# Performance work log

Measured on AMD Instinct MI355X. Metric: run time of the kernel, lower is better.

The kernel has to match this reference:

```python
import jax, jax.numpy as jnp
import numpy as np

B, L, DS, DP = 4, 384, 384, 128
NEAR_BAND = 4
LN_EPS = 1e-5


def setup_inputs():
    key = jax.random.key(0)
    k = jax.random.split(key, 16)
    return {
        "seq_repr": jax.random.normal(k[0], (B, L, DS), jnp.float32),
        "pair_repr": jax.random.normal(k[1], (B, L, L, DP), jnp.float32),
        "ln_s_g": 1.0 + 0.1 * jax.random.normal(k[2], (DS,), jnp.float32),
        "ln_s_b": 0.1 * jax.random.normal(k[3], (DS,), jnp.float32),
        "ln_z_g": 1.0 + 0.1 * jax.random.normal(k[4], (DP,), jnp.float32),
        "ln_z_b": 0.1 * jax.random.normal(k[5], (DP,), jnp.float32),
        "W_seq": jax.random.normal(k[6], (DS, DS), jnp.float32) / np.sqrt(DS).astype(np.float32),
        "W_pair": jax.random.normal(k[7], (DP, DP), jnp.float32) / np.sqrt(DP).astype(np.float32),
        "W_gs": 0.02 * jax.random.normal(k[8], (2 * DS, DS), jnp.float32),
        "b_gs": jnp.ones((DS,), jnp.float32),
        "W_gz": 0.02 * jax.random.normal(k[9], (2 * DP, DP), jnp.float32),
        "b_gz": jnp.ones((DP,), jnp.float32),
        "W1": jax.random.normal(k[10], (DS + 2 * DP, 64), jnp.float32) / np.sqrt(DS + 2 * DP).astype(np.float32),
        "b1": 0.01 * jax.random.normal(k[11], (64,), jnp.float32),
        "W2": jax.random.normal(k[12], (64, 1), jnp.float32) / 8.0,
        "b2": jnp.zeros((1,), jnp.float32),
        "chain_id": jax.random.randint(k[13], (B, L), 0, 2, jnp.int32),
        "mask": jax.random.randint(k[14], (B, L), 0, 2, jnp.int32).astype(jnp.bool_),
    }


def _layernorm(x, g, b):
    mu = jnp.mean(x, axis=-1, keepdims=True)
    var = jnp.mean(jnp.square(x - mu), axis=-1, keepdims=True)
    return (x - mu) * jax.lax.rsqrt(var + LN_EPS) * g + b


def _masked_mean(x, m, axes):
    num = jnp.sum(x * m, axis=axes)
    den = jnp.clip(jnp.sum(m, axis=axes), 1e-6, None)  # mask has trailing dim 1 -> den broadcasts
    return num / den


def _masked_max(x, m, axis):
    v = jnp.max(jnp.where(m > 0, x, -jnp.inf), axis=axis)
    return jnp.where(jnp.isinf(v), jnp.zeros_like(v), v)


def reference(seq_repr, pair_repr, ln_s_g, ln_s_b, ln_z_g, ln_z_b, W_seq, W_pair,
              W_gs, b_gs, W_gz, b_gz, W1, b1, W2, b2, chain_id, mask):
    # sequence branch: LN -> Linear -> masked mean/max over L -> gated blend
    s = _layernorm(seq_repr, ln_s_g, ln_s_b) @ W_seq          # [B,L,DS]
    m = mask.astype(s.dtype)[..., None]                        # [B,L,1]
    s_mean = _masked_mean(s, m, 1)                             # [B,DS]
    s_max = _masked_max(s, m, 1)                               # [B,DS]
    gate_s = jax.nn.sigmoid(jnp.concatenate([s_max, s_mean], -1) @ W_gs + b_gs)
    s_feat = s_mean + gate_s * (s_max - s_mean)

    # pair branch: symmetrize, zero diagonal, LN -> Linear
    p = 0.5 * (pair_repr + jnp.swapaxes(pair_repr, 1, 2))      # [B,L,L,DP]
    eye = jnp.eye(L, dtype=p.dtype)[None, :, :, None]
    p = p * (1.0 - eye)
    p = _layernorm(p, ln_z_g, ln_z_b) @ W_pair

    pm = (mask[:, :, None] & mask[:, None, :])[..., None].astype(p.dtype)   # [B,L,L,1]
    same = (chain_id[:, :, None] == chain_id[:, None, :])[..., None]
    intra = pm * same.astype(p.dtype)
    inter = pm * (~same).astype(p.dtype)

    inter_mean = _masked_mean(p, inter, (1, 2))                # [B,DP]
    row_den = jnp.clip(jnp.sum(inter, axis=2), 1e-6, None)     # [B,L,1]
    row_mean = jnp.sum(p * inter, axis=2) / row_den            # [B,L,DP]
    inter_peak = jnp.max(row_mean, axis=1)                     # [B,DP]
    gate_z = jax.nn.sigmoid(jnp.concatenate([inter_peak, inter_mean], -1) @ W_gz + b_gz)
    inter_feat = inter_mean + gate_z * (inter_peak - inter_mean)

    idx = jnp.arange(L)
    band = (jnp.abs(idx[:, None] - idx[None, :]) <= NEAR_BAND)[None, :, :, None].astype(p.dtype)
    intra_compact = _masked_mean(p, intra * band, (1, 2))      # [B,DP]

    feat = jnp.concatenate([s_feat, inter_feat, intra_compact], -1)  # [B, DS+2*DP]
    h = jax.nn.relu(feat @ W1 + b1)
    prob = jax.nn.sigmoid(h @ W2 + b2)[..., 0]                 # [B]
    return prob
```

## Files before the change

kernel.cpp:

```cpp
#include <hip/hip_runtime.h>
#include <math.h>

#define B_  4
#define L_  384
#define DS_ 384
#define DP_ 128
#define NB_ 4
#define FEAT_ (DS_ + 2*DP_)
#define LN_EPS_ 1e-5f
#define T_ 16
#define NT_ (L_ / T_)
#define NTP_ (NT_ * (NT_ + 1) / 2)
#define SROWS_ 4

__device__ __forceinline__ int detect_mode_block(const void* __restrict__ raw) {
    const unsigned int* dw = (const unsigned int*)raw;
    int li = 1, lf = 1;
    for (int i = threadIdx.x; i < (B_ * L_) / 4; i += blockDim.x) {
        unsigned int v = dw[i];
        if (v != 0u && v != 1u) li = 0;
        if (v != 0u && v != 0x3F800000u) lf = 0;
    }
    int ai = __syncthreads_and(li);
    int af = __syncthreads_and(lf);
    return ai ? 0 : (af ? 1 : 2);
}
__device__ __forceinline__ int mask_at(const void* __restrict__ raw, int mode, int idx) {
    if (mode == 0) return ((const unsigned int*)raw)[idx] != 0u;
    if (mode == 1) return ((const float*)raw)[idx] != 0.0f;
    return ((const unsigned char*)raw)[idx] != 0;
}

__device__ __forceinline__ size_t poff(int b, int tile, int slot, int row) {
    return ((((size_t)b * NT_ + tile) * NT_ + slot) * T_ + row) * DP_;
}
__device__ __forceinline__ size_t pdoff(int b, int tile, int slot, int row) {
    return (((size_t)b * NT_ + tile) * NT_ + slot) * T_ + row;
}

__global__ __launch_bounds__(256) void k_pair_tiles(
    const float* __restrict__ pair, const float* __restrict__ gz,
    const float* __restrict__ bz, const int* __restrict__ chain,
    const void* __restrict__ mask_raw,
    float* __restrict__ PI, float* __restrict__ PA,
    float* __restrict__ PDI, float* __restrict__ PDA) {
    __shared__ float smJI[T_][DP_], smJA[T_][DP_];
    __shared__ float smDJI[T_], smDJA[T_];
    __shared__ int s_m[2 * T_], s_c[2 * T_];

    const int mode = detect_mode_block(mask_raw);

    const int b = blockIdx.x / NTP_;
    int t = blockIdx.x % NTP_;
    int ta = 0;
    while (t >= NT_ - ta) { t -= NT_ - ta; ta++; }
    const int tb = ta + t;
    const int i0 = ta * T_, j0 = tb * T_;
    const float fac = (ta == tb) ? 0.5f : 1.0f;

    const int tid = threadIdx.x;
    const int wave = tid >> 6, lane = tid & 63;
    const int ch2 = lane * 2;

    for (int idx = tid; idx < T_ * DP_; idx += 256) {
        (&smJI[0][0])[idx] = 0.f;
        (&smJA[0][0])[idx] = 0.f;
    }
    if (tid < T_) { smDJI[tid] = 0.f; smDJA[tid] = 0.f; }
    if (tid < 2 * T_) {
        const int loc = (tid < T_) ? (i0 + tid) : (j0 + tid - T_);
        s_m[tid] = mask_at(mask_raw, mode, b * L_ + loc);
        s_c[tid] = chain[b * L_ + loc];
    }
    __syncthreads();

    const float g0 = gz[ch2], g1 = gz[ch2 + 1];
    const float bb0 = bz[ch2], bb1 = bz[ch2 + 1];
    const float* baseb = pair + (size_t)b * L_ * L_ * DP_;

    float accI0[4] = {0, 0, 0, 0}, accI1[4] = {0, 0, 0, 0};
    float accA0[4] = {0, 0, 0, 0}, accA1[4] = {0, 0, 0, 0};
    float denI[4] = {0, 0, 0, 0}, denA[4] = {0, 0, 0, 0};

    for (int r = 0; r < 4; ++r) {
        const int il = (wave << 2) + r;
        const int gi = i0 + il;
        if (!s_m[il]) continue;
        const int ci = s_c[il];
        for (int jl = 0; jl < T_; ++jl) {
            if (!s_m[T_ + jl]) continue;
            const int gj = j0 + jl;
            const bool same = (s_c[T_ + jl] == ci);
            int d = gi - gj; d = d < 0 ? -d : d;
            const float wI = (!same) ? fac : 0.f;
            const float wA = (same && d <= NB_) ? fac : 0.f;
            if (wI == 0.f && wA == 0.f) continue;
            float v0, v1;
            if (gi == gj) {
                v0 = 0.f; v1 = 0.f;
            } else {
                const float2 a = *(const float2*)(baseb + ((size_t)gi * L_ + gj) * DP_ + ch2);
                const float2 c = *(const float2*)(baseb + ((size_t)gj * L_ + gi) * DP_ + ch2);
                v0 = 0.5f * (a.x + c.x); v1 = 0.5f * (a.y + c.y);
            }
            float s = v0 + v1, q = v0 * v0 + v1 * v1;
            #pragma unroll
            for (int off = 32; off; off >>= 1) {
                s += __shfl_xor(s, off);
                q += __shfl_xor(q, off);
            }
            const float mu = s * (1.f / DP_);
            const float rstd = rsqrtf(q * (1.f / DP_) - mu * mu + LN_EPS_);
            const float y0 = (v0 - mu) * rstd * g0 + bb0;
            const float y1 = (v1 - mu) * rstd * g1 + bb1;
            accI0[r] += wI * y0; accI1[r] += wI * y1;
            accA0[r] += wA * y0; accA1[r] += wA * y1;
            denI[r] += wI; denA[r] += wA;
            if (wI != 0.f) {
                atomicAdd(&smJI[jl][ch2], wI * y0);
                atomicAdd(&smJI[jl][ch2 + 1], wI * y1);
                if (lane == 0) atomicAdd(&smDJI[jl], wI);
            }
            if (wA != 0.f) {
                atomicAdd(&smJA[jl][ch2], wA * y0);
                atomicAdd(&smJA[jl][ch2 + 1], wA * y1);
                if (lane == 0) atomicAdd(&smDJA[jl], wA);
            }
        }
    }
    __syncthreads();

    if (ta != tb) {
        #pragma unroll
        for (int r = 0; r < 4; ++r) {
            const int il = (wave << 2) + r;
            const size_t o = poff(b, ta, tb, il) + ch2;
            PI[o] = accI0[r]; PI[o + 1] = accI1[r];
            PA[o] = accA0[r]; PA[o + 1] = accA1[r];
            if (lane == 0) {
                PDI[pdoff(b, ta, tb, il)] = denI[r];
                PDA[pdoff(b, ta, tb, il)] = denA[r];
            }
        }
        for (int idx = tid; idx < T_ * DP_; idx += 256) {
            const int jl = idx >> 7, ch = idx & 127;
            const size_t o = poff(b, tb, ta, jl) + ch;
            PI[o] = smJI[jl][ch];
            PA[o] = smJA[jl][ch];
        }
        if (tid < T_) {
            PDI[pdoff(b, tb, ta, tid)] = smDJI[tid];
            PDA[pdoff(b, tb, ta, tid)] = smDJA[tid];
        }
    } else {
        #pragma unroll
        for (int r = 0; r < 4; ++r) {
            const int il = (wave << 2) + r;
            const size_t o = poff(b, ta, ta, il) + ch2;
            PI[o] = accI0[r] + smJI[il][ch2];
            PI[o + 1] = accI1[r] + smJI[il][ch2 + 1];
            PA[o] = accA0[r] + smJA[il][ch2];
            PA[o + 1] = accA1[r] + smJA[il][ch2 + 1];
            if (lane == 0) {
                PDI[pdoff(b, ta, ta, il)] = denI[r] + smDJI[il];
                PDA[pdoff(b, ta, ta, il)] = denA[r] + smDJA[il];
            }
        }
    }
}

__global__ __launch_bounds__(384) void k_seq_proj(
    const float* __restrict__ seq, const float* __restrict__ gs,
    const float* __restrict__ bs, const float* __restrict__ W,
    float* __restrict__ s_rows) {
    const int row0 = blockIdx.x * SROWS_;
    const int tid = threadIdx.x;
    const int wave = tid >> 6, lane = tid & 63;
    __shared__ float xn[SROWS_][DS_];
    __shared__ float sSum[SROWS_][6], sSq[SROWS_][6];
    const float gg = gs[tid], bbv = bs[tid];
    #pragma unroll
    for (int r = 0; r < SROWS_; r++) {
        float x = seq[(size_t)(row0 + r) * DS_ + tid];
        float s = x, q = x * x;
        #pragma unroll
        for (int off = 32; off; off >>= 1) {
            s += __shfl_xor(s, off);
            q += __shfl_xor(q, off);
        }
        if (lane == 0) { sSum[r][wave] = s; sSq[r][wave] = q; }
        xn[r][tid] = x;
    }
    __syncthreads();
    float mu[SROWS_], rstd[SROWS_];
    #pragma unroll
    for (int r = 0; r < SROWS_; r++) {
        float ts = 0.f, tq = 0.f;
        #pragma unroll
        for (int w = 0; w < 6; w++) { ts += sSum[r][w]; tq += sSq[r][w]; }
        mu[r] = ts * (1.0f / DS_);
        float var = tq * (1.0f / DS_) - mu[r] * mu[r];
        rstd[r] = rsqrtf(var + LN_EPS_);
    }
    #pragma unroll
    for (int r = 0; r < SROWS_; r++)
        xn[r][tid] = (xn[r][tid] - mu[r]) * rstd[r] * gg + bbv;
    __syncthreads();
    float acc[SROWS_] = {0.f, 0.f, 0.f, 0.f};
    for (int k = 0; k < DS_; k++) {
        float w = W[(size_t)k * DS_ + tid];
        #pragma unroll
        for (int r = 0; r < SROWS_; r++) acc[r] += xn[r][k] * w;
    }
    #pragma unroll
    for (int r = 0; r < SROWS_; r++)
        s_rows[(size_t)(row0 + r) * DS_ + tid] = acc[r];
}

__global__ __launch_bounds__(384) void k_mid(
    const float* __restrict__ s_rows, const void* __restrict__ mask_raw,
    const float* __restrict__ Wp,
    const float* __restrict__ PI, const float* __restrict__ PA,
    const float* __restrict__ PDI, const float* __restrict__ PDA,
    float* __restrict__ psum, float* __restrict__ pmax, int* __restrict__ pcnt,
    float* __restrict__ pI, float* __restrict__ pA, float* __restrict__ pPk,
    float* __restrict__ pdI, float* __restrict__ pdA) {
    __shared__ float sWp[DP_ * DP_];
    __shared__ float sRS[DP_];
    const int tid = threadIdx.x;

    if (blockIdx.x < B_ * NT_) {
        const int b = blockIdx.x / NT_, tile = blockIdx.x % NT_;
        for (int i = tid; i < DP_ * DP_; i += 384) sWp[i] = Wp[i];
        __syncthreads();
        float totI = 0.f, totA = 0.f, dI = 0.f, dA = 0.f, peak = -INFINITY;
        for (int r = 0; r < T_; ++r) {
            float dr = 0.f;
            if (tid < DP_) {
                float rsI = 0.f, rsA = 0.f, da = 0.f;
                const size_t o0 = poff(b, tile, 0, r) + tid;
                const size_t d0 = pdoff(b, tile, 0, r);
                #pragma unroll 4
                for (int s = 0; s < NT_; ++s) {
                    rsI += PI[o0 + (size_t)s * T_ * DP_];
                    rsA += PA[o0 + (size_t)s * T_ * DP_];
                    dr += PDI[d0 + (size_t)s * T_];
                    da += PDA[d0 + (size_t)s * T_];
                }
                sRS[tid] = rsI;
                totI += rsI; totA += rsA; dI += dr; dA += da;
            }
            __syncthreads();
            if (tid < DP_) {
                float acc = 0.f;
                #pragma unroll 8
                for (int k = 0; k < DP_; ++k) acc += sRS[k] * sWp[(k << 7) + tid];
                peak = fmaxf(peak, acc / fmaxf(dr, 1e-6f));
            }
            __syncthreads();
        }
        if (tid < DP_) {
            pI[(size_t)(b * NT_ + tile) * DP_ + tid] = totI;
            pA[(size_t)(b * NT_ + tile) * DP_ + tid] = totA;
            pPk[(size_t)(b * NT_ + tile) * DP_ + tid] = peak;
            if (tid == 0) { pdI[b * NT_ + tile] = dI; pdA[b * NT_ + tile] = dA; }
        }
    } else {
        const int bi = blockIdx.x - B_ * NT_;
        const int b = bi / NT_, tile = bi % NT_;
        const int mode = detect_mode_block(mask_raw);
        float sum = 0.f, mx = -INFINITY;
        int cnt = 0;
        const int l0 = tile * T_;
        for (int l = l0; l < l0 + T_; ++l) {
            if (mask_at(mask_raw, mode, b * L_ + l)) {
                float v = s_rows[(size_t)(b * L_ + l) * DS_ + tid];
                sum += v; mx = fmaxf(mx, v); cnt++;
            }
        }
        psum[(size_t)(b * NT_ + tile) * DS_ + tid] = sum;
        pmax[(size_t)(b * NT_ + tile) * DS_ + tid] = mx;
        if (tid == 0) pcnt[b * NT_ + tile] = cnt;
    }
}

__global__ __launch_bounds__(384) void k_finalize(
    const float* __restrict__ psum, const float* __restrict__ pmax,
    const int* __restrict__ pcnt,
    const float* __restrict__ pI, const float* __restrict__ pA,
    const float* __restrict__ pPk,
    const float* __restrict__ pdI, const float* __restrict__ pdA,
    const float* __restrict__ Wgs, const float* __restrict__ bgs,
    const float* __restrict__ Wp, const float* __restrict__ Wgz,
    const float* __restrict__ bgz,
    const float* __restrict__ W1, const float* __restrict__ b1,
    const float* __restrict__ W2, const float* __restrict__ b2,
    float* __restrict__ out) {
    const int b = blockIdx.x;
    const int tid = threadIdx.x;
    __shared__ float sMean[DS_], sMax[DS_], fI[DP_], fA[DP_], sPk[DP_], sIM[DP_];
    __shared__ float feat[FEAT_];
    __shared__ float sdI, sdA;
    {
        float s = 0.f, m = -INFINITY;
        int cnt = 0;
        for (int c = 0; c < NT_; ++c) {
            s += psum[(size_t)(b * NT_ + c) * DS_ + tid];
            m = fmaxf(m, pmax[(size_t)(b * NT_ + c) * DS_ + tid]);
            cnt += pcnt[b * NT_ + c];
        }
        sMean[tid] = s / fmaxf((float)cnt, 1e-6f);
        sMax[tid] = (cnt > 0) ? m : 0.f;
    }
    if (tid < DP_) {
        float tI = 0.f, tA = 0.f, pk = -INFINITY, ddI = 0.f, ddA = 0.f;
        for (int c = 0; c < NT_; ++c) {
            tI += pI[(size_t)(b * NT_ + c) * DP_ + tid];
            tA += pA[(size_t)(b * NT_ + c) * DP_ + tid];
            pk = fmaxf(pk, pPk[(size_t)(b * NT_ + c) * DP_ + tid]);
            ddI += pdI[b * NT_ + c]; ddA += pdA[b * NT_ + c];
        }
        fI[tid] = tI; fA[tid] = tA; sPk[tid] = pk;
        if (tid == 0) { sdI = ddI; sdA = ddA; }
    }
    __syncthreads();
    {
        float acc = bgs[tid];
        #pragma unroll 4
        for (int k = 0; k < DS_; ++k)
            acc += sMax[k] * Wgs[(size_t)k * DS_ + tid]
                 + sMean[k] * Wgs[(size_t)(k + DS_) * DS_ + tid];
        const float gate = 1.f / (1.f + expf(-acc));
        feat[tid] = sMean[tid] + gate * (sMax[tid] - sMean[tid]);
    }
    if (tid < DP_) {
        float aI = 0.f, aA = 0.f;
        #pragma unroll 4
        for (int k = 0; k < DP_; ++k) {
            aI += fI[k] * Wp[(k << 7) + tid];
            aA += fA[k] * Wp[(k << 7) + tid];
        }
        sIM[tid] = aI / fmaxf(sdI, 1e-6f);
        feat[DS_ + DP_ + tid] = aA / fmaxf(sdA, 1e-6f);
    }
    __syncthreads();
    if (tid < DP_) {
        float acc = bgz[tid];
        #pragma unroll 4
        for (int k = 0; k < DP_; ++k)
            acc += sPk[k] * Wgz[(k << 7) + tid] + sIM[k] * Wgz[((k + DP_) << 7) + tid];
        const float gate = 1.f / (1.f + expf(-acc));
        feat[DS_ + tid] = sIM[tid] + gate * (sPk[tid] - sIM[tid]);
    }
    __syncthreads();
    if (tid < 64) {
        float acc = b1[tid];
        #pragma unroll 4
        for (int k = 0; k < FEAT_; ++k) acc += feat[k] * W1[(k << 6) + tid];
        float p = fmaxf(acc, 0.f) * W2[tid];
        #pragma unroll
        for (int off = 32; off; off >>= 1) p += __shfl_xor(p, off);
        if (tid == 0) out[b] = 1.f / (1.f + expf(-(p + b2[0])));
    }
}

extern "C" void kernel_launch(void* const* d_in, const int* in_sizes, int n_in,
                              void* d_out, int out_size, void* d_ws, size_t ws_size,
                              hipStream_t stream) {
    const float* seq    = (const float*)d_in[0];
    const float* pair   = (const float*)d_in[1];
    const float* ln_s_g = (const float*)d_in[2];
    const float* ln_s_b = (const float*)d_in[3];
    const float* ln_z_g = (const float*)d_in[4];
    const float* ln_z_b = (const float*)d_in[5];
    const float* W_seq  = (const float*)d_in[6];
    const float* W_pair = (const float*)d_in[7];
    const float* W_gs   = (const float*)d_in[8];
    const float* b_gs   = (const float*)d_in[9];
    const float* W_gz   = (const float*)d_in[10];
    const float* b_gz   = (const float*)d_in[11];
    const float* W1     = (const float*)d_in[12];
    const float* b1     = (const float*)d_in[13];
    const float* W2     = (const float*)d_in[14];
    const float* b2     = (const float*)d_in[15];
    const int*   chain  = (const int*)d_in[16];
    const void*  mask   = d_in[17];
    float* out = (float*)d_out;

    char* ws = (char*)d_ws;
    const size_t nP  = (size_t)B_ * NT_ * NT_ * T_ * DP_;
    const size_t nPD = (size_t)B_ * NT_ * NT_ * T_;
    float* PI  = (float*)ws;  ws += nP * 4;
    float* PA  = (float*)ws;  ws += nP * 4;
    float* PDI = (float*)ws;  ws += nPD * 4;
    float* PDA = (float*)ws;  ws += nPD * 4;
    float* s_rows = (float*)ws; ws += (size_t)B_ * L_ * DS_ * 4;
    float* psum = (float*)ws;   ws += (size_t)B_ * NT_ * DS_ * 4;
    float* pmax = (float*)ws;   ws += (size_t)B_ * NT_ * DS_ * 4;
    int*   pcnt = (int*)ws;     ws += (size_t)B_ * NT_ * 4;
    float* pI   = (float*)ws;   ws += (size_t)B_ * NT_ * DP_ * 4;
    float* pA   = (float*)ws;   ws += (size_t)B_ * NT_ * DP_ * 4;
    float* pPk  = (float*)ws;   ws += (size_t)B_ * NT_ * DP_ * 4;
    float* pdI  = (float*)ws;   ws += (size_t)B_ * NT_ * 4;
    float* pdA  = (float*)ws;   ws += (size_t)B_ * NT_ * 4;

    k_seq_proj<<<(B_ * L_) / SROWS_, 384, 0, stream>>>(seq, ln_s_g, ln_s_b, W_seq, s_rows);
    k_pair_tiles<<<B_ * NTP_, 256, 0, stream>>>(pair, ln_z_g, ln_z_b, chain, mask,
                                                PI, PA, PDI, PDA);
    k_mid<<<2 * B_ * NT_, 384, 0, stream>>>(s_rows, mask, W_pair, PI, PA, PDI, PDA,
                                            psum, pmax, pcnt, pI, pA, pPk, pdI, pdA);
    k_finalize<<<B_, 384, 0, stream>>>(psum, pmax, pcnt, pI, pA, pPk, pdI, pdA,
                                       W_gs, b_gs, W_pair, W_gz, b_gz,
                                       W1, b1, W2, b2, out);
}
```

Baseline: 655.3 us.

## Merge seq projection into pair-tile kernel and batch eligible pair loads via ballot

Combines the sequence LayerNorm+projection and the pair-tile reduction into one launch, with extra blocks handling sequence rows (now 8 rows per 256-thread block). In the pair path, a wave ballot precomputes which (i,j) pairs are eligible, so the loop iterates only those and issues up to four pairs' global loads before their LayerNorm reductions, for more memory-level parallelism. Diagonal tiles now fold row accumulators through shared atomics. The aim is to remove a launch, let the two independent workloads overlap on the GPU, and hide pair-load latency, at the cost of more registers and larger unrolled code.

```diff
diff --git a/kernel.cpp b/kernel.cpp
--- a/kernel.cpp
+++ b/kernel.cpp
@@ -11,7 +11,7 @@
 #define T_ 16
 #define NT_ (L_ / T_)
 #define NTP_ (NT_ * (NT_ + 1) / 2)
-#define SROWS_ 4
+#define SQROWS_ 8
 
 __device__ __forceinline__ int detect_mode_block(const void* __restrict__ raw) {
     const unsigned int* dw = (const unsigned int*)raw;
@@ -38,110 +38,162 @@
     return (((size_t)b * NT_ + tile) * NT_ + slot) * T_ + row;
 }
 
-__global__ __launch_bounds__(256) void k_pair_tiles(
+#define WREDUCE2(S, Q) do { \
+    (S) += __shfl_xor((S), 32); (Q) += __shfl_xor((Q), 32); \
+    (S) += __shfl_xor((S), 16); (Q) += __shfl_xor((Q), 16); \
+    (S) += __shfl_xor((S), 8);  (Q) += __shfl_xor((Q), 8);  \
+    (S) += __shfl_xor((S), 4);  (Q) += __shfl_xor((Q), 4);  \
+    (S) += __shfl_xor((S), 2);  (Q) += __shfl_xor((Q), 2);  \
+    (S) += __shfl_xor((S), 1);  (Q) += __shfl_xor((Q), 1);  \
+} while (0)
+
+#define LNACC(JL, AA, CC) do { \
+    const int gj_ = j0 + (JL); \
+    const bool same_ = (s_c[T_ + (JL)] == ci); \
+    int dd_ = gi - gj_; dd_ = dd_ < 0 ? -dd_ : dd_; \
+    const float wI_ = same_ ? 0.f : fac; \
+    const float wA_ = (same_ && dd_ <= NB_) ? fac : 0.f; \
+    float v0_, v1_; \
+    if (gi == gj_) { v0_ = 0.f; v1_ = 0.f; } \
+    else { v0_ = 0.5f * ((AA).x + (CC).x); v1_ = 0.5f * ((AA).y + (CC).y); } \
+    float s_ = v0_ + v1_, q_ = v0_ * v0_ + v1_ * v1_; \
+    WREDUCE2(s_, q_); \
+    const float mu_ = s_ * (1.f / DP_); \
+    const float rstd_ = rsqrtf(q_ * (1.f / DP_) - mu_ * mu_ + LN_EPS_); \
+    const float y0_ = (v0_ - mu_) * rstd_ * g0 + bb0; \
+    const float y1_ = (v1_ - mu_) * rstd_ * g1 + bb1; \
+    aI0 += wI_ * y0_; aI1 += wI_ * y1_; \
+    aA0 += wA_ * y0_; aA1 += wA_ * y1_; \
+    adI += wI_; adA += wA_; \
+    if (wI_ != 0.f) { \
+        atomicAdd(&smJI[JL][ch2], wI_ * y0_); \
+        atomicAdd(&smJI[JL][ch2 + 1], wI_ * y1_); \
+        if (lane == 0) atomicAdd(&smDJI[JL], wI_); \
+    } \
+    if (wA_ != 0.f) { \
+        atomicAdd(&smJA[JL][ch2], wA_ * y0_); \
+        atomicAdd(&smJA[JL][ch2 + 1], wA_ * y1_); \
+        if (lane == 0) atomicAdd(&smDJA[JL], wA_); \
+    } \
+} while (0)
+
+__global__ __launch_bounds__(256) void k_main(
     const float* __restrict__ pair, const float* __restrict__ gz,
     const float* __restrict__ bz, const int* __restrict__ chain,
     const void* __restrict__ mask_raw,
+    const float* __restrict__ seq, const float* __restrict__ gs,
+    const float* __restrict__ bs, const float* __restrict__ Wseq,
     float* __restrict__ PI, float* __restrict__ PA,
-    float* __restrict__ PDI, float* __restrict__ PDA) {
-    __shared__ float smJI[T_][DP_], smJA[T_][DP_];
-    __shared__ float smDJI[T_], smDJA[T_];
-    __shared__ int s_m[2 * T_], s_c[2 * T_];
-
-    const int mode = detect_mode_block(mask_raw);
-
-    const int b = blockIdx.x / NTP_;
-    int t = blockIdx.x % NTP_;
-    int ta = 0;
-    while (t >= NT_ - ta) { t -= NT_ - ta; ta++; }
-    const int tb = ta + t;
-    const int i0 = ta * T_, j0 = tb * T_;
-    const float fac = (ta == tb) ? 0.5f : 1.0f;
-
+    float* __restrict__ PDI, float* __restrict__ PDA,
+    float* __restrict__ s_rows) {
+    __shared__ __align__(16) float shraw[4200];
     const int tid = threadIdx.x;
     const int wave = tid >> 6, lane = tid & 63;
-    const int ch2 = lane * 2;
-
-    for (int idx = tid; idx < T_ * DP_; idx += 256) {
-        (&smJI[0][0])[idx] = 0.f;
-        (&smJA[0][0])[idx] = 0.f;
-    }
-    if (tid < T_) { smDJI[tid] = 0.f; smDJA[tid] = 0.f; }
-    if (tid < 2 * T_) {
-        const int loc = (tid < T_) ? (i0 + tid) : (j0 + tid - T_);
-        s_m[tid] = mask_at(mask_raw, mode, b * L_ + loc);
-        s_c[tid] = chain[b * L_ + loc];
-    }
-    __syncthreads();
-
-    const float g0 = gz[ch2], g1 = gz[ch2 + 1];
-    const float bb0 = bz[ch2], bb1 = bz[ch2 + 1];
-    const float* baseb = pair + (size_t)b * L_ * L_ * DP_;
-
-    float accI0[4] = {0, 0, 0, 0}, accI1[4] = {0, 0, 0, 0};
-    float accA0[4] = {0, 0, 0, 0}, accA1[4] = {0, 0, 0, 0};
-    float denI[4] = {0, 0, 0, 0}, denA[4] = {0, 0, 0, 0};
-
-    for (int r = 0; r < 4; ++r) {
-        const int il = (wave << 2) + r;
-        const int gi = i0 + il;
-        if (!s_m[il]) continue;
-        const int ci = s_c[il];
-        for (int jl = 0; jl < T_; ++jl) {
-            if (!s_m[T_ + jl]) continue;
-            const int gj = j0 + jl;
-            const bool same = (s_c[T_ + jl] == ci);
-            int d = gi - gj; d = d < 0 ? -d : d;
-            const float wI = (!same) ? fac : 0.f;
-            const float wA = (same && d <= NB_) ? fac : 0.f;
-            if (wI == 0.f && wA == 0.f) continue;
-            float v0, v1;
-            if (gi == gj) {
-                v0 = 0.f; v1 = 0.f;
-            } else {
-                const float2 a = *(const float2*)(baseb + ((size_t)gi * L_ + gj) * DP_ + ch2);
-                const float2 c = *(const float2*)(baseb + ((size_t)gj * L_ + gi) * DP_ + ch2);
-                v0 = 0.5f * (a.x + c.x); v1 = 0.5f * (a.y + c.y);
-            }
-            float s = v0 + v1, q = v0 * v0 + v1 * v1;
-            #pragma unroll
-            for (int off = 32; off; off >>= 1) {
-                s += __shfl_xor(s, off);
-                q += __shfl_xor(q, off);
-            }
-            const float mu = s * (1.f / DP_);
-            const float rstd = rsqrtf(q * (1.f / DP_) - mu * mu + LN_EPS_);
-            const float y0 = (v0 - mu) * rstd * g0 + bb0;
-            const float y1 = (v1 - mu) * rstd * g1 + bb1;
-            accI0[r] += wI * y0; accI1[r] += wI * y1;
-            accA0[r] += wA * y0; accA1[r] += wA * y1;
-            denI[r] += wI; denA[r] += wA;
-            if (wI != 0.f) {
-                atomicAdd(&smJI[jl][ch2], wI * y0);
-                atomicAdd(&smJI[jl][ch2 + 1], wI * y1);
-                if (lane == 0) atomicAdd(&smDJI[jl], wI);
-            }
-            if (wA != 0.f) {
-                atomicAdd(&smJA[jl][ch2], wA * y0);
-                atomicAdd(&smJA[jl][ch2 + 1], wA * y1);
-                if (lane == 0) atomicAdd(&smDJA[jl], wA);
-            }
-        }
-    }
-    __syncthreads();
-
-    if (ta != tb) {
+
+    if (blockIdx.x < B_ * NTP_) {
+        float (*smJI)[DP_] = (float(*)[DP_])shraw;
+        float (*smJA)[DP_] = (float(*)[DP_])(shraw + 2048);
+        float* smDJI = shraw + 4096;
+        float* smDJA = shraw + 4112;
+        int* s_m = (int*)(shraw + 4128);
+        int* s_c = (int*)(shraw + 4160);
+
+        const int mode = detect_mode_block(mask_raw);
+
+        const int b = blockIdx.x / NTP_;
+        int t = blockIdx.x % NTP_;
+        int ta = 0;
+        while (t >= NT_ - ta) { t -= NT_ - ta; ta++; }
+        const int tb = ta + t;
+        const int i0 = ta * T_, j0 = tb * T_;
+        const float fac = (ta == tb) ? 0.5f : 1.0f;
+        const int ch2 = lane * 2;
+
+        for (int idx = tid; idx < T_ * DP_; idx += 256) {
+            (&smJI[0][0])[idx] = 0.f;
+            (&smJA[0][0])[idx] = 0.f;
+        }
+        if (tid < T_) { smDJI[tid] = 0.f; smDJA[tid] = 0.f; }
+        if (tid < 2 * T_) {
+            const int loc = (tid < T_) ? (i0 + tid) : (j0 + tid - T_);
+            s_m[tid] = mask_at(mask_raw, mode, b * L_ + loc);
+            s_c[tid] = chain[b * L_ + loc];
+        }
+        __syncthreads();
+
+        const float g0 = gz[ch2], g1 = gz[ch2 + 1];
+        const float bb0 = bz[ch2], bb1 = bz[ch2 + 1];
+        const float* baseb = pair + (size_t)b * L_ * L_ * DP_;
+
+        unsigned long long elig;
+        {
+            const int r_ = lane >> 4, jl_ = lane & 15;
+            const int il_ = (wave << 2) + r_;
+            bool e = s_m[il_] && s_m[T_ + jl_];
+            if (e) {
+                const bool same = (s_c[T_ + jl_] == s_c[il_]);
+                int dd = (i0 + il_) - (j0 + jl_); dd = dd < 0 ? -dd : dd;
+                e = (!same) || (dd <= NB_);
+            }
+            elig = __ballot(e);
+        }
+
         #pragma unroll
         for (int r = 0; r < 4; ++r) {
             const int il = (wave << 2) + r;
-            const size_t o = poff(b, ta, tb, il) + ch2;
-            PI[o] = accI0[r]; PI[o + 1] = accI1[r];
-            PA[o] = accA0[r]; PA[o + 1] = accA1[r];
-            if (lane == 0) {
-                PDI[pdoff(b, ta, tb, il)] = denI[r];
-                PDA[pdoff(b, ta, tb, il)] = denA[r];
-            }
-        }
+            const int gi = i0 + il;
+            const int ci = s_c[il];
+            float aI0 = 0.f, aI1 = 0.f, aA0 = 0.f, aA1 = 0.f, adI = 0.f, adA = 0.f;
+            unsigned int mr = (unsigned int)((elig >> (r * 16)) & 0xFFFFull);
+            while (mr) {
+                int ja = __ffs(mr) - 1; mr &= mr - 1;
+                int jb = -1, jc = -1, jd = -1;
+                if (mr) { jb = __ffs(mr) - 1; mr &= mr - 1; }
+                if (mr) { jc = __ffs(mr) - 1; mr &= mr - 1; }
+                if (mr) { jd = __ffs(mr) - 1; mr &= mr - 1; }
+                float2 Aa = make_float2(0.f, 0.f), Ca = Aa, Ab = Aa, Cb = Aa;
+                float2 Ac = Aa, Cc = Aa, Ad = Aa, Cd = Aa;
+                if (gi != j0 + ja) {
+                    Aa = *(const float2*)(baseb + ((size_t)gi * L_ + (j0 + ja)) * DP_ + ch2);
+                    Ca = *(const float2*)(baseb + ((size_t)(j0 + ja) * L_ + gi) * DP_ + ch2);
+                }
+                if (jb >= 0 && gi != j0 + jb) {
+                    Ab = *(const float2*)(baseb + ((size_t)gi * L_ + (j0 + jb)) * DP_ + ch2);
+                    Cb = *(const float2*)(baseb + ((size_t)(j0 + jb) * L_ + gi) * DP_ + ch2);
+                }
+                if (jc >= 0 && gi != j0 + jc) {
+                    Ac = *(const float2*)(baseb + ((size_t)gi * L_ + (j0 + jc)) * DP_ + ch2);
+                    Cc = *(const float2*)(baseb + ((size_t)(j0 + jc) * L_ + gi) * DP_ + ch2);
+                }
+                if (jd >= 0 && gi != j0 + jd) {
+                    Ad = *(const float2*)(baseb + ((size_t)gi * L_ + (j0 + jd)) * DP_ + ch2);
+                    Cd = *(const float2*)(baseb + ((size_t)(j0 + jd) * L_ + gi) * DP_ + ch2);
+                }
+                LNACC(ja, Aa, Ca);
+                if (jb >= 0) LNACC(jb, Ab, Cb);
+                if (jc >= 0) LNACC(jc, Ac, Cc);
+                if (jd >= 0) LNACC(jd, Ad, Cd);
+            }
+            if (ta != tb) {
+                const size_t o = poff(b, ta, tb, il) + ch2;
+                PI[o] = aI0; PI[o + 1] = aI1;
+                PA[o] = aA0; PA[o + 1] = aA1;
+                if (lane == 0) {
+                    PDI[pdoff(b, ta, tb, il)] = adI;
+                    PDA[pdoff(b, ta, tb, il)] = adA;
+                }
+            } else {
+                atomicAdd(&smJI[il][ch2], aI0);
+                atomicAdd(&smJI[il][ch2 + 1], aI1);
+                atomicAdd(&smJA[il][ch2], aA0);
+                atomicAdd(&smJA[il][ch2 + 1], aA1);
+                if (lane == 0) {
+                    atomicAdd(&smDJI[il], adI);
+                    atomicAdd(&smDJA[il], adA);
+                }
+            }
+        }
+        __syncthreads();
         for (int idx = tid; idx < T_ * DP_; idx += 256) {
             const int jl = idx >> 7, ch = idx & 127;
             const size_t o = poff(b, tb, ta, jl) + ch;
@@ -153,68 +205,59 @@
             PDA[pdoff(b, tb, ta, tid)] = smDJA[tid];
         }
     } else {
-        #pragma unroll
-        for (int r = 0; r < 4; ++r) {
-            const int il = (wave << 2) + r;
-            const size_t o = poff(b, ta, ta, il) + ch2;
-            PI[o] = accI0[r] + smJI[il][ch2];
-            PI[o + 1] = accI1[r] + smJI[il][ch2 + 1];
-            PA[o] = accA0[r] + smJA[il][ch2];
-            PA[o + 1] = accA1[r] + smJA[il][ch2 + 1];
-            if (lane == 0) {
-                PDI[pdoff(b, ta, ta, il)] = denI[r] + smDJI[il];
-                PDA[pdoff(b, ta, ta, il)] = denA[r] + smDJA[il];
-            }
-        }
-    }
-}
-
-__global__ __launch_bounds__(384) void k_seq_proj(
-    const float* __restrict__ seq, const float* __restrict__ gs,
-    const float* __restrict__ bs, const float* __restrict__ W,
-    float* __restrict__ s_rows) {
-    const int row0 = blockIdx.x * SROWS_;
-    const int tid = threadIdx.x;
-    const int wave = tid >> 6, lane = tid & 63;
-    __shared__ float xn[SROWS_][DS_];
-    __shared__ float sSum[SROWS_][6], sSq[SROWS_][6];
-    const float gg = gs[tid], bbv = bs[tid];
-    #pragma unroll
-    for (int r = 0; r < SROWS_; r++) {
-        float x = seq[(size_t)(row0 + r) * DS_ + tid];
-        float s = x, q = x * x;
-        #pragma unroll
-        for (int off = 32; off; off >>= 1) {
-            s += __shfl_xor(s, off);
-            q += __shfl_xor(q, off);
-        }
-        if (lane == 0) { sSum[r][wave] = s; sSq[r][wave] = q; }
-        xn[r][tid] = x;
-    }
-    __syncthreads();
-    float mu[SROWS_], rstd[SROWS_];
-    #pragma unroll
-    for (int r = 0; r < SROWS_; r++) {
-        float ts = 0.f, tq = 0.f;
-        #pragma unroll
-        for (int w = 0; w < 6; w++) { ts += sSum[r][w]; tq += sSq[r][w]; }
-        mu[r] = ts * (1.0f / DS_);
-        float var = tq * (1.0f / DS_) - mu[r] * mu[r];
-        rstd[r] = rsqrtf(var + LN_EPS_);
-    }
-    #pragma unroll
-    for (int r = 0; r < SROWS_; r++)
-        xn[r][tid] = (xn[r][tid] - mu[r]) * rstd[r] * gg + bbv;
-    __syncthreads();
-    float acc[SROWS_] = {0.f, 0.f, 0.f, 0.f};
-    for (int k = 0; k < DS_; k++) {
-        float w = W[(size_t)k * DS_ + tid];
-        #pragma unroll
-        for (int r = 0; r < SROWS_; r++) acc[r] += xn[r][k] * w;
-    }
-    #pragma unroll
-    for (int r = 0; r < SROWS_; r++)
-        s_rows[(size_t)(row0 + r) * DS_ + tid] = acc[r];
+        float (*xn)[DS_] = (float(*)[DS_])shraw;
+        float* red = shraw + 3072;
+        const int sb = blockIdx.x - B_ * NTP_;
+        const int row0 = sb * SQROWS_;
+        const float gg0 = gs[tid], bv0 = bs[tid];
+        float gg1 = 0.f, bv1 = 0.f;
+        if (tid < 128) { gg1 = gs[256 + tid]; bv1 = bs[256 + tid]; }
+
+        #pragma unroll
+        for (int r = 0; r < SQROWS_; ++r) {
+            const float* xr = seq + (size_t)(row0 + r) * DS_;
+            const float x0 = xr[tid];
+            const float x1 = (tid < 128) ? xr[256 + tid] : 0.f;
+            float s = x0 + x1, q = x0 * x0 + x1 * x1;
+            WREDUCE2(s, q);
+            if (lane == 0) { red[r * 4 + wave] = s; red[32 + r * 4 + wave] = q; }
+            xn[r][tid] = x0;
+            if (tid < 128) xn[r][256 + tid] = x1;
+        }
+        __syncthreads();
+        float muv[SQROWS_], rsv[SQROWS_];
+        #pragma unroll
+        for (int r = 0; r < SQROWS_; ++r) {
+            const float ts = red[r * 4] + red[r * 4 + 1] + red[r * 4 + 2] + red[r * 4 + 3];
+            const float tq = red[32 + r * 4] + red[32 + r * 4 + 1] + red[32 + r * 4 + 2] + red[32 + r * 4 + 3];
+            muv[r] = ts * (1.f / DS_);
+            rsv[r] = rsqrtf(tq * (1.f / DS_) - muv[r] * muv[r] + LN_EPS_);
+        }
+        __syncthreads();
+        #pragma unroll
+        for (int r = 0; r < SQROWS_; ++r) {
+            xn[r][tid] = (xn[r][tid] - muv[r]) * rsv[r] * gg0 + bv0;
+            if (tid < 128) xn[r][256 + tid] = (xn[r][256 + tid] - muv[r]) * rsv[r] * gg1 + bv1;
+        }
+        __syncthreads();
+        float acc0[SQROWS_] = {0.f, 0.f, 0.f, 0.f, 0.f, 0.f, 0.f, 0.f};
+        float acc1[SQROWS_] = {0.f, 0.f, 0.f, 0.f, 0.f, 0.f, 0.f, 0.f};
+        for (int k = 0; k < DS_; ++k) {
+            const float w0 = Wseq[(size_t)k * DS_ + tid];
+            const float w1 = (tid < 128) ? Wseq[(size_t)k * DS_ + 256 + tid] : 0.f;
+            #pragma unroll
+            for (int r = 0; r < SQROWS_; ++r) {
+                const float xk = xn[r][k];
+                acc0[r] += xk * w0;
+                acc1[r] += xk * w1;
+            }
+        }
+        #pragma unroll
+        for (int r = 0; r < SQROWS_; ++r) {
+            s_rows[(size_t)(row0 + r) * DS_ + tid] = acc0[r];
+            if (tid < 128) s_rows[(size_t)(row0 + r) * DS_ + 256 + tid] = acc1[r];
+        }
+    }
 }
 
 __global__ __launch_bounds__(384) void k_mid(
@@ -404,9 +447,10 @@
     float* pdI  = (float*)ws;   ws += (size_t)B_ * NT_ * 4;
     float* pdA  = (float*)ws;   ws += (size_t)B_ * NT_ * 4;
 
-    k_seq_proj<<<(B_ * L_) / SROWS_, 384, 0, stream>>>(seq, ln_s_g, ln_s_b, W_seq, s_rows);
-    k_pair_tiles<<<B_ * NTP_, 256, 0, stream>>>(pair, ln_z_g, ln_z_b, chain, mask,
-                                                PI, PA, PDI, PDA);
+    const int seqBlocks = (B_ * L_) / SQROWS_;
+    k_main<<<B_ * NTP_ + seqBlocks, 256, 0, stream>>>(
+        pair, ln_z_g, ln_z_b, chain, mask, seq, ln_s_g, ln_s_b, W_seq,
+        PI, PA, PDI, PDA, s_rows);
     k_mid<<<2 * B_ * NT_, 384, 0, stream>>>(s_rows, mask, W_pair, PI, PA, PDI, PDA,
                                             psum, pmax, pcnt, pI, pA, pPk, pdI, pdA);
     k_finalize<<<B_, 384, 0, stream>>>(psum, pmax, pcnt, pI, pA, pPk, pdI, pdA,
```

After: 647.8 us. No clear change (-1.1%).
